# Kernel tuning notes

Measured on AMD Instinct MI355X. Metric: run time of the kernel, lower is better.

## Reference

```python
import jax
import jax.numpy as jnp
import numpy as np
from jax import lax

DIM = 512
B, T = 8, 2048
DT = 1.0
DT_REF = 1.0
MAX_GROWTH = 0.3


def _xavier(key, shape):
    fan_in, fan_out = shape[1], shape[0]
    lim = float(np.sqrt(6.0 / (fan_in + fan_out)))
    return jax.random.uniform(key, shape, jnp.float32, -lim, lim)


def setup_inputs() -> dict:
    key = jax.random.key(0)
    ks = jax.random.split(key, 10)
    D = DIM
    return {
        "x": jax.random.normal(ks[0], (B, T, D), jnp.float32),
        # ComplexSVDTransform params (U basis is unused by the transform matrix)
        "v_raw_re": jax.random.normal(ks[1], (D, D), jnp.float32) * 0.02,
        "v_raw_im": jax.random.normal(ks[2], (D, D), jnp.float32) * 0.02,
        "log_sigma": jnp.zeros((D,), jnp.float32),
        "dft_weight": jnp.zeros((), jnp.float32),
        # GlobalFluxTracker params (gate_net only used in forward_step; not here)
        "decay_re": jax.random.normal(ks[3], (D,), jnp.float32) * 0.1 - 1.0,
        "decay_im": jax.random.normal(ks[4], (D,), jnp.float32) * 0.1,
        "mix_w": _xavier(ks[5], (2 * D, 2 * D)),
        "mix_b": jnp.zeros((2 * D,), jnp.float32),
        "proj_w": _xavier(ks[6], (2 * D, 2 * D)),
        "proj_b": jnp.zeros((2 * D,), jnp.float32),
        # TemporalPropagator eigenvalue params
        "lam_re": jax.random.normal(ks[7], (D,), jnp.float32) * 0.01,
        "lam_im": jax.random.normal(ks[8], (D,), jnp.float32) * 0.1,
    }


def _cayley(raw_re, raw_im):
    # Q = (I + A_skew)^{-1} (I - A_skew), A_skew = A - A^H
    A = raw_re + 1j * raw_im
    A_skew = A - A.conj().T
    I = jnp.eye(A.shape[0], dtype=A.dtype)
    return jnp.linalg.solve(I + A_skew, I - A_skew)


def _transform_matrix(v_raw_re, v_raw_im, log_sigma, dft_weight):
    V = _cayley(v_raw_re, v_raw_im)
    S = jnp.exp(log_sigma)
    d = v_raw_re.shape[0]
    n = jnp.arange(d, dtype=jnp.float32)
    k = n[:, None]
    dft = jnp.exp(-2j * jnp.pi * (n * k) / d) / jnp.sqrt(jnp.asarray(d, jnp.float32))
    alpha = jax.nn.sigmoid(dft_weight).astype(jnp.complex64)
    V_scaled = V * S[None, :].astype(V.dtype)  # V @ diag(S)
    return V_scaled * (1.0 - alpha) + dft.astype(jnp.complex64) * alpha


def _scan_combine(c1, c2):
    # s_t = a_t * s_{t-1} + b_t  -> associative combine (later element is c2)
    a1, b1 = c1
    a2, b2 = c2
    return (a1 * a2, b1 * a2 + b2)


def reference(x, v_raw_re, v_raw_im, log_sigma, dft_weight,
              decay_re, decay_im, mix_w, mix_b, proj_w, proj_b,
              lam_re, lam_im):
    D = x.shape[-1]
    # --- encode ---
    W = _transform_matrix(v_raw_re, v_raw_im, log_sigma, dft_weight)  # [D,D] complex
    h = jnp.einsum('btd,de->bte', x.astype(jnp.complex64), W)  # [B,T,D] complex
    # --- flux tracker operators ---
    decay = jax.nn.sigmoid(decay_re) + 1j * decay_im  # [D]
    x_cat = jnp.concatenate([h.real, h.imag], axis=-1)  # [B,T,2D]
    x_in = x_cat @ mix_w.T + mix_b
    x_re, x_im = x_in[..., :D], x_in[..., D:]
    X = x_re + 1j * x_im  # forcing [B,T,D]
    A = jnp.broadcast_to(decay.astype(jnp.complex64), h.shape)  # [B,T,D]
    # --- complex diagonal SSM recurrence via parallel scan ---
    _, states = lax.associative_scan(_scan_combine, (A, X.astype(jnp.complex64)), axis=1)
    # --- project states to source ---
    s_cat = jnp.concatenate([states.real, states.imag], axis=-1)
    s_out = s_cat @ proj_w.T + proj_b
    source = s_out[..., :D] + 1j * s_out[..., D:]
    # --- closed-form transition operators ---
    lam = jnp.clip(lam_re, -MAX_GROWTH, MAX_GROWTH) + 1j * lam_im  # [D]
    exp_arg = lam * (DT / DT_REF)
    t_decay = jnp.exp(exp_arg)
    lam_safe = lam + 1e-8 * jnp.sign(lam.real + 1e-12)
    forcing = (jnp.exp(exp_arg) - 1.0) / lam_safe
    h_out = h * t_decay + source * forcing  # [B,T,D]
    # --- decode ---
    W_inv = jnp.linalg.inv(W)
    x_out = jnp.einsum('btd,de->bte', h_out, W_inv)
    return x_out.real


if __name__ == "__main__":
    out = reference(**setup_inputs())
    print(out.shape, out.dtype)
```

## Files before the change

### kernel.cpp

```cpp
#include <hip/hip_runtime.h>
#include <hip/hip_bf16.h>

typedef unsigned short u16;
typedef _Float16 f16x8 __attribute__((ext_vector_type(8)));
typedef float f32x4 __attribute__((ext_vector_type(4)));

#define DEV __device__ __forceinline__

DEV u16 f2h(float f) { _Float16 h = (_Float16)f; u16 u; __builtin_memcpy(&u, &h, 2); return u; }
DEV float h2f(u16 u) { _Float16 h; __builtin_memcpy(&h, &u, 2); return (float)h; }
DEV void splitf(float v, u16& hi, u16& lo) { hi = f2h(v); lo = f2h(v - h2f(hi)); }
DEV float sigm(float x) { return 1.f / (1.f + __expf(-x)); }
DEV void gload16(const u16* g, u16* l) {
  __builtin_amdgcn_global_load_lds((const __attribute__((address_space(1))) void*)g,
                                   (__attribute__((address_space(3))) void*)l, 16, 0, 0);
}

static const int TT = 2048;

static const size_t OFF_AUGF   = 0;
static const size_t OFF_AUG    = OFF_AUGF   + (size_t)512*512*8;
static const size_t OFF_BINV   = OFF_AUG    + (size_t)512*512*16;
static const size_t OFF_PIV    = OFF_BINV   + (size_t)64*64*16;
static const size_t OFF_MCOPY  = OFF_PIV    + (size_t)64*512*16;
static const size_t OFF_TAB    = OFF_MCOPY  + (size_t)512*64*16;
static const size_t OFF_WCATH  = OFF_TAB    + (size_t)512*32;
static const size_t OFF_WCATL  = OFF_WCATH  + (size_t)512*1024*2;
static const size_t OFF_MIXH   = OFF_WCATL  + (size_t)512*1024*2;
static const size_t OFF_MIXL   = OFF_MIXH   + (size_t)1024*1024*2;
static const size_t OFF_PROJH  = OFF_MIXL   + (size_t)1024*1024*2;
static const size_t OFF_PROJL  = OFF_PROJH  + (size_t)1024*1024*2;
static const size_t OFF_B1TH   = OFF_PROJL  + (size_t)1024*1024*2;
static const size_t OFF_B1TL   = OFF_B1TH   + (size_t)512*1024*2;
static const size_t OFF_B2TH   = OFF_B1TL   + (size_t)512*1024*2;
static const size_t OFF_B2TL   = OFF_B2TH   + (size_t)512*1024*2;
static const size_t OFF_BTMIXH = OFF_B2TL   + (size_t)512*1024*2;
static const size_t OFF_BTMIXL = OFF_BTMIXH + (size_t)1024*512*2;
static const size_t OFF_BTFH   = OFF_BTMIXL + (size_t)1024*512*2;
static const size_t OFF_BTFL   = OFF_BTFH   + (size_t)512*1536*2;
static const size_t OFF_BIAS2  = OFF_BTFL   + (size_t)512*1536*2;
static const size_t OFF_CARRY  = OFF_BIAS2  + (size_t)512*4;
static const size_t OFF_PREF   = OFF_CARRY  + (size_t)4096*16*8;
static const size_t OFF_XINF   = OFF_PREF   + (size_t)4096*16*8;
static const size_t OFF_ACATH  = OFF_XINF   + (size_t)16384*1024*4;
static const size_t OFF_ACATL  = OFF_ACATH  + (size_t)16384*1536*2;

__global__ __launch_bounds__(256) void k_split_f32(const float* __restrict__ s, u16* __restrict__ dh,
                                                   u16* __restrict__ dl, int n4) {
  int g = blockIdx.x * 256 + threadIdx.x;
  if (g >= n4) return;
  float4 v = ((const float4*)s)[g];
  ushort4 h, l;
  splitf(v.x, h.x, l.x); splitf(v.y, h.y, l.y); splitf(v.z, h.z, l.z); splitf(v.w, h.w, l.w);
  ((ushort4*)dh)[g] = h;
  ((ushort4*)dl)[g] = l;
}

__global__ __launch_bounds__(256) void k_x_to_acat(const float* __restrict__ x, u16* __restrict__ ah,
                                                   u16* __restrict__ al) {
  int g = blockIdx.x * 256 + threadIdx.x;
  if (g >= 2097152) return;
  float4 v = ((const float4*)x)[g];
  int idx = g * 4;
  int row = idx >> 9, col = idx & 511;
  ushort4 h, l;
  splitf(v.x, h.x, l.x); splitf(v.y, h.y, l.y); splitf(v.z, h.z, l.z); splitf(v.w, h.w, l.w);
  *(ushort4*)(ah + (size_t)row*1536 + col) = h;
  *(ushort4*)(al + (size_t)row*1536 + col) = l;
}

__global__ __launch_bounds__(256) void k_transpose_1024(const float* __restrict__ in, u16* __restrict__ oh,
                                                        u16* __restrict__ ol) {
  __shared__ float s[64][65];
  int lx = threadIdx.x & 63, ly = threadIdx.x >> 6;
#pragma unroll
  for (int i = 0; i < 16; ++i) {
    int c = blockIdx.y*64 + ly*16 + i;
    s[ly*16 + i][lx] = in[(size_t)c*1024 + blockIdx.x*64 + lx];
  }
  __syncthreads();
#pragma unroll
  for (int i = 0; i < 16; ++i) {
    int j = blockIdx.x*64 + ly*16 + i;
    u16 h, l; splitf(s[lx][ly*16 + i], h, l);
    oh[(size_t)j*1024 + blockIdx.y*64 + lx] = h;
    ol[(size_t)j*1024 + blockIdx.y*64 + lx] = l;
  }
}

__global__ __launch_bounds__(256) void k_build_aug_f(const float* __restrict__ vre, const float* __restrict__ vim,
                                                     float2* __restrict__ aug) {
  int g = blockIdx.x * 256 + threadIdx.x;
  if (g >= 512*512) return;
  int i = g >> 9, j = g & 511;
  float sre = vre[i*512 + j] - vre[j*512 + i];
  float sim = vim[i*512 + j] + vim[j*512 + i];
  float idd = (i == j) ? 1.f : 0.f;
  aug[g] = make_float2(idd + sre, sim);
}

template<typename T2, typename TR>
__global__ __launch_bounds__(1024) void gj_inv64_p(const T2* __restrict__ AUG, T2* __restrict__ BINV,
                                                   T2* __restrict__ MCOPY, int k0) {
  if (blockIdx.x > 0) {
    int b = blockIdx.x - 1;
    for (int l = threadIdx.x; l < 4096; l += 1024) {
      int rr = l >> 6, cc = l & 63;
      MCOPY[(size_t)(b*64 + rr)*64 + cc] = AUG[(size_t)(b*64 + rr)*512 + k0 + cc];
    }
    return;
  }
  __shared__ T2 mcol[2][64];
  __shared__ T2 praw[2][68];
  const int tid = threadIdx.x;
  const int r = tid >> 4, q = tid & 15;
  T2 a[4];
  const T2* src = AUG + (size_t)(k0 + r)*512 + k0 + q*4;
#pragma unroll
  for (int jj = 0; jj < 4; ++jj) a[jj] = src[jj];
  if (q == 0) mcol[0][r] = a[0];
  if (r == 0) {
#pragma unroll
    for (int jj = 0; jj < 4; ++jj) { int j = q*4 + jj; praw[0][j + (j >> 4)] = a[jj]; }
  }
  __syncthreads();
  for (int p = 0; p < 64; ++p) {
    const int bu = p & 1;
    T2 pd = praw[bu][p + (p >> 4)];
    TR inv = TR(1) / (pd.x*pd.x + pd.y*pd.y);
    T2 pinv; pinv.x = pd.x*inv; pinv.y = -pd.y*inv;
    T2 mraw = mcol[bu][r];
    T2 g; g.x = mraw.x*pinv.x - mraw.y*pinv.y; g.y = mraw.x*pinv.y + mraw.y*pinv.x;
    if (r == p) {
#pragma unroll
      for (int jj = 0; jj < 4; ++jj) {
        int j = q*4 + jj;
        T2 v;
        if (j == p) v = pinv;
        else { T2 pr = praw[bu][j + (j >> 4)]; v.x = pr.x*pinv.x - pr.y*pinv.y; v.y = pr.x*pinv.y + pr.y*pinv.x; }
        a[jj] = v;
      }
    } else {
#pragma unroll
      for (int jj = 0; jj < 4; ++jj) {
        int j = q*4 + jj;
        if (j == p) { a[jj].x = -g.x; a[jj].y = -g.y; }
        else {
          T2 pr = praw[bu][j + (j >> 4)];
          a[jj].x -= g.x*pr.x - g.y*pr.y;
          a[jj].y -= g.x*pr.y + g.y*pr.x;
        }
      }
    }
    if (p < 63) {
      const int nbu = bu ^ 1;
      if (q == ((p + 1) >> 2)) {
        const int loc = (p + 1) & 3;
#pragma unroll
        for (int jj = 0; jj < 4; ++jj) if (jj == loc) mcol[nbu][r] = a[jj];
      }
      if (r == p + 1) {
#pragma unroll
        for (int jj = 0; jj < 4; ++jj) { int j = q*4 + jj; praw[nbu][j + (j >> 4)] = a[jj]; }
      }
    }
    __syncthreads();
  }
  T2* dst = BINV + (size_t)r*64 + q*4;
#pragma unroll
  for (int jj = 0; jj < 4; ++jj) dst[jj] = a[jj];
}

template<typename T2>
__global__ __launch_bounds__(256) void gj_trans_t(const T2* __restrict__ AUG, const T2* __restrict__ BINV,
                                                  T2* __restrict__ PIV, int k0, int s) {
  __shared__ T2 binv[64][16];
  int tid = threadIdx.x;
  int cj = blockIdx.x + (blockIdx.x >= s ? 1 : 0);
  int col = cj*64 + (tid & 63);
  int rsub = tid >> 6;
  T2 acc[16];
#pragma unroll
  for (int i = 0; i < 16; ++i) { acc[i].x = 0; acc[i].y = 0; }
  for (int kc = 0; kc < 4; ++kc) {
    for (int l = tid; l < 1024; l += 256) {
      int rr = l >> 4, cc = l & 15;
      binv[rr][cc] = BINV[(size_t)rr*64 + kc*16 + cc];
    }
    __syncthreads();
#pragma unroll 4
    for (int kk = 0; kk < 16; ++kk) {
      T2 av = AUG[(size_t)(k0 + kc*16 + kk)*512 + col];
#pragma unroll
      for (int i = 0; i < 16; ++i) {
        T2 bv = binv[rsub*16 + i][kk];
        acc[i].x += bv.x*av.x - bv.y*av.y;
        acc[i].y += bv.x*av.y + bv.y*av.x;
      }
    }
    __syncthreads();
  }
#pragma unroll
  for (int i = 0; i < 16; ++i) PIV[(size_t)(rsub*16 + i)*512 + col] = acc[i];
}

template<typename T2>
__global__ __launch_bounds__(256) void gj_update_t(T2* __restrict__ AUG, const T2* __restrict__ PIV,
                                                   const T2* __restrict__ BINV, const T2* __restrict__ MCOPY,
                                                   int k0) {
  __shared__ T2 mult[16][64];
  __shared__ T2 pivc[16][64];
  int tid = threadIdx.x;
  int rb = blockIdx.y;
  int cj = blockIdx.x;
  const int s = k0 >> 6;
  const bool ispiv = (cj == s);
  int colBase = cj*64;
  for (int l = tid; l < 1024; l += 256) {
    int rr = l >> 6, kk = l & 63;
    mult[rr][kk] = MCOPY[(size_t)(rb*16 + rr)*64 + kk];
  }
  int ccl = tid & 63, rsub = tid >> 6;
  int col = colBase + ccl;
  T2 acc[4];
  if (ispiv) {
#pragma unroll
    for (int i = 0; i < 4; ++i) { acc[i].x = 0; acc[i].y = 0; }
  } else {
#pragma unroll
    for (int i = 0; i < 4; ++i) acc[i] = AUG[(size_t)(rb*16 + rsub*4 + i)*512 + col];
  }
  for (int kc = 0; kc < 4; ++kc) {
    for (int l = tid; l < 1024; l += 256) {
      int rr = l >> 6, cc = l & 63;
      pivc[rr][cc] = ispiv ? BINV[(size_t)(kc*16 + rr)*64 + cc]
                           : PIV[(size_t)(kc*16 + rr)*512 + colBase + cc];
    }
    __syncthreads();
#pragma unroll 4
    for (int k2 = 0; k2 < 16; ++k2) {
      T2 pv = pivc[k2][ccl];
#pragma unroll
      for (int i = 0; i < 4; ++i) {
        T2 m = mult[rsub*4 + i][kc*16 + k2];
        acc[i].x -= m.x*pv.x - m.y*pv.y;
        acc[i].y -= m.x*pv.y + m.y*pv.x;
      }
    }
    __syncthreads();
  }
#pragma unroll
  for (int i = 0; i < 4; ++i) {
    int gr = rb*16 + rsub*4 + i;
    T2 o = acc[i];
    if (gr >= k0 && gr < k0 + 64) {
      o = ispiv ? BINV[(size_t)(gr - k0)*64 + ccl] : PIV[(size_t)(gr - k0)*512 + col];
    }
    AUG[(size_t)gr*512 + col] = o;
  }
}

__global__ __launch_bounds__(256) void k_build_w(const float2* __restrict__ augf, const float* __restrict__ lsig,
                                                 const float* __restrict__ dw, double2* __restrict__ w64,
                                                 u16* __restrict__ wch, u16* __restrict__ wcl) {
  int g = blockIdx.x * 256 + threadIdx.x;
  if (g >= 512*512) return;
  int k = g >> 9, j = g & 511;
  float2 Z = augf[(size_t)k*512 + j];
  double Vre = 2.0*(double)Z.x - ((k == j) ? 1.0 : 0.0);
  double Vim = 2.0*(double)Z.y;
  double S = exp((double)lsig[j]);
  double al = 1.0 / (1.0 + exp(-(double)dw[0]));
  double sc = S * (1.0 - al);
  const float n2pi = (float)(-2.0 * 3.14159265358979323846);
  float nk = (float)(k * j);
  float ph32 = (n2pi * nk) / 512.0f;
  double sn, cs; sincos((double)ph32, &sn, &cs);
  float snf = (float)sn, csf = (float)cs;
  float rsq = sqrtf(512.0f);
  float dre = csf / rsq;
  float dimv = snf / rsq;
  double2 w = make_double2(Vre*sc + (double)dre*al, Vim*sc + (double)dimv*al);
  w64[(size_t)k*512 + j] = w;
  u16 h, l;
  splitf((float)w.x, h, l);
  wch[(size_t)k*1024 + j] = h;  wcl[(size_t)k*1024 + j] = l;
  splitf((float)w.y, h, l);
  wch[(size_t)k*1024 + 512 + j] = h;  wcl[(size_t)k*1024 + 512 + j] = l;
}

__global__ __launch_bounds__(256) void k_const512(const float* __restrict__ lamre, const float* __restrict__ lamim,
                                                  double4* __restrict__ tab) {
  int g = blockIdx.x * 256 + threadIdx.x;
  if (g >= 512) return;
  double lr = fmin(fmax((double)lamre[g], -0.3), 0.3);
  double li = (double)lamim[g];
  double e = exp(lr);
  double sn, cs; sincos(li, &sn, &cs);
  double tdre = e*cs, tdim = e*sn;
  double sgn = (lr + 1e-12) >= 0.0 ? 1.0 : -1.0;
  double lsr = lr + 1e-8*sgn, lsi = li;
  double numr = tdre - 1.0, numi = tdim;
  double idn = 1.0 / (lsr*lsr + lsi*lsi);
  double fr = (numr*lsr + numi*lsi)*idn;
  double fi = (numi*lsr - numr*lsi)*idn;
  tab[g] = make_double4(tdre, tdim, fr, fi);
}

__global__ __launch_bounds__(256) void k_build_tb(const double2* __restrict__ winv, const double4* __restrict__ tab,
                                                  u16* __restrict__ b1h, u16* __restrict__ b1l,
                                                  u16* __restrict__ b2h, u16* __restrict__ b2l) {
  int g = blockIdx.x * 256 + threadIdx.x;
  if (g >= 512*512) return;
  int e = g & 511, m = g >> 9;
  double2 wv = winv[(size_t)m*512 + e];
  double4 tb = tab[m];
  double twre = tb.x*wv.x - tb.y*wv.y, twim = tb.x*wv.y + tb.y*wv.x;
  double fwre = tb.z*wv.x - tb.w*wv.y, fwim = tb.z*wv.y + tb.w*wv.x;
  u16 h, l;
  splitf((float)twre, h, l);  b1h[(size_t)e*1024 + m] = h;        b1l[(size_t)e*1024 + m] = l;
  splitf((float)-twim, h, l); b1h[(size_t)e*1024 + 512 + m] = h;  b1l[(size_t)e*1024 + 512 + m] = l;
  splitf((float)fwre, h, l);  b2h[(size_t)e*1024 + m] = h;        b2l[(size_t)e*1024 + m] = l;
  splitf((float)-fwim, h, l); b2h[(size_t)e*1024 + 512 + m] = h;  b2l[(size_t)e*1024 + 512 + m] = l;
}

__global__ __launch_bounds__(256) void k_bias2(const double2* __restrict__ winv, const double4* __restrict__ tab,
                                               const float* __restrict__ projb, float* __restrict__ bias2) {
  int e = blockIdx.x;
  int t = threadIdx.x;
  double acc = 0.0;
  for (int d = t; d < 512; d += 256) {
    double2 wv = winv[(size_t)d*512 + e];
    double4 tb = tab[d];
    double fwre = tb.z*wv.x - tb.w*wv.y;
    double fwim = tb.z*wv.y + tb.w*wv.x;
    acc += (double)projb[d]*fwre - (double)projb[512 + d]*fwim;
  }
#pragma unroll
  for (int off = 32; off; off >>= 1) acc += __shfl_down(acc, off, 64);
  __shared__ double red[4];
  if ((t & 63) == 0) red[t >> 6] = acc;
  __syncthreads();
  if (t == 0) bias2[e] = (float)(red[0] + red[1] + red[2] + red[3]);
}

template<int K, int NOUT, int EPI, int LDA, int LDO>
__global__ __launch_bounds__(256) void gemm3(const u16* __restrict__ Ah, const u16* __restrict__ Al,
                                             const u16* __restrict__ Bh, const u16* __restrict__ Bl,
                                             u16* __restrict__ outH, u16* __restrict__ outL,
                                             float* __restrict__ outF, const float* __restrict__ bias) {
  __shared__ alignas(16) u16 Ash[128*64];
  __shared__ alignas(16) u16 Asl[128*64];
  __shared__ alignas(16) u16 Bsh[128*64];
  __shared__ alignas(16) u16 Bsl[128*64];
  const int tid = threadIdx.x;
  const int lane = tid & 63, wid = tid >> 6;
  const int wr = wid >> 1, wc = wid & 1;
  const int nwg = gridDim.x * gridDim.y;
  const int flatb = blockIdx.y * gridDim.x + blockIdx.x;
  const int chunk = nwg >> 3;
  const int swz = (flatb & 7) * chunk + (flatb >> 3);
  const int rowTile = (swz / gridDim.x) * 128;
  const int colTile = (swz % gridDim.x) * 128;
  f32x4 zz = {0.f, 0.f, 0.f, 0.f};
  f32x4 acc[4][4];
#pragma unroll
  for (int m = 0; m < 4; ++m)
#pragma unroll
    for (int n = 0; n < 4; ++n) acc[m][n] = zz;

  const int KT = K / 64;
  for (int kt = 0; kt < KT; ++kt) {
    const int k0 = kt * 64;
    __syncthreads();
#pragma unroll
    for (int i = 0; i < 4; ++i) {
      int flat = i*256 + tid;
      int ar = flat >> 3;
      int as = (flat & 7) ^ (ar & 7);
      size_t aoff = (size_t)(rowTile + ar)*LDA + (k0 + as*8);
      size_t boff = (size_t)(colTile + ar)*K   + (k0 + as*8);
      int lb = (i*256 + (tid & ~63)) * 8;
      gload16(Ah + aoff, Ash + lb);
      gload16(Al + aoff, Asl + lb);
      gload16(Bh + boff, Bsh + lb);
      gload16(Bl + boff, Bsl + lb);
    }
    __syncthreads();
#pragma unroll
    for (int ks = 0; ks < 2; ++ks) {
      f16x8 afh[4], afl[4], bfh[4], bfl[4];
#pragma unroll
      for (int m = 0; m < 4; ++m) {
        int row = wr*64 + m*16 + (lane & 15);
        int off = row*128 + (((ks*4 + (lane >> 4)) ^ (row & 7)) << 4);
        afh[m] = *(const f16x8*)((const char*)Ash + off);
        afl[m] = *(const f16x8*)((const char*)Asl + off);
      }
#pragma unroll
      for (int n = 0; n < 4; ++n) {
        int row = wc*64 + n*16 + (lane & 15);
        int off = row*128 + (((ks*4 + (lane >> 4)) ^ (row & 7)) << 4);
        bfh[n] = *(const f16x8*)((const char*)Bsh + off);
        bfl[n] = *(const f16x8*)((const char*)Bsl + off);
      }
#pragma unroll
      for (int m = 0; m < 4; ++m)
#pragma unroll
        for (int n = 0; n < 4; ++n) {
          acc[m][n] = __builtin_amdgcn_mfma_f32_16x16x32_f16(afl[m], bfh[n], acc[m][n], 0, 0, 0);
          acc[m][n] = __builtin_amdgcn_mfma_f32_16x16x32_f16(afh[m], bfl[n], acc[m][n], 0, 0, 0);
          acc[m][n] = __builtin_amdgcn_mfma_f32_16x16x32_f16(afh[m], bfh[n], acc[m][n], 0, 0, 0);
        }
    }
  }
  const int colBase = colTile + wc*64;
  const int rowBase = rowTile + wr*64 + (lane >> 4)*4;
#pragma unroll
  for (int n = 0; n < 4; ++n) {
    int col = colBase + n*16 + (lane & 15);
    float bv = (EPI >= 2) ? bias[col] : 0.f;
#pragma unroll
    for (int m = 0; m < 4; ++m) {
#pragma unroll
      for (int j = 0; j < 4; ++j) {
        int row = rowBase + m*16 + j;
        float v = acc[m][n][j] + bv;
        if (EPI >= 2) {
          outF[(size_t)row*LDO + col] = v;
        } else {
          u16 h, l; splitf(v, h, l);
          outH[(size_t)row*LDO + col] = h;
          outL[(size_t)row*LDO + col] = l;
        }
      }
    }
  }
}

__global__ __launch_bounds__(256) void k_scan1(const float* __restrict__ xin, const float* __restrict__ dre_,
                                               const float* __restrict__ dim_, float2* __restrict__ carry) {
  int g = blockIdx.x * 256 + threadIdx.x;
  int d = g & 511; int rr = g >> 9; int b = rr & 7; int c = rr >> 3;
  float dre = sigm(dre_[d]);
  float dim = dim_[d];
  size_t base = ((size_t)(b*TT + c*128))*1024 + d;
  float sre = 0.f, sim = 0.f;
  for (int t = 0; t < 128; ++t) {
    float xre = xin[base];
    float xim = xin[base + 512];
    float nre = dre*sre - dim*sim + xre;
    float nim = dre*sim + dim*sre + xim;
    sre = nre; sim = nim;
    base += 1024;
  }
  carry[((size_t)(b*512 + d))*16 + c] = make_float2(sre, sim);
}

__global__ __launch_bounds__(256) void k_scan2(const float* __restrict__ dre_, const float* __restrict__ dim_,
                                               const float2* __restrict__ carry, float2* __restrict__ pref) {
  int g = blockIdx.x * 256 + threadIdx.x;
  int d = g & 511; int b = g >> 9;
  float dre = sigm(dre_[d]);
  float dim = dim_[d];
  float are = dre, aim = dim;
#pragma unroll
  for (int i = 0; i < 7; ++i) { float nr = are*are - aim*aim; float ni = 2.f*are*aim; are = nr; aim = ni; }
  float sre = 0.f, sim = 0.f;
  size_t base = ((size_t)(b*512 + d))*16;
  for (int c = 0; c < 16; ++c) {
    pref[base + c] = make_float2(sre, sim);
    float2 cr = carry[base + c];
    float nr = are*sre - aim*sim + cr.x;
    float ni = are*sim + aim*sre + cr.y;
    sre = nr; sim = ni;
  }
}

__global__ __launch_bounds__(256) void k_scan3(const float* __restrict__ xin, const float* __restrict__ dre_,
                                               const float* __restrict__ dim_, const float2* __restrict__ pref,
                                               u16* __restrict__ ah, u16* __restrict__ al) {
  int g = blockIdx.x * 256 + threadIdx.x;
  int d = g & 511; int rr = g >> 9; int b = rr & 7; int c = rr >> 3;
  float dre = sigm(dre_[d]);
  float dim = dim_[d];
  float2 p0 = pref[((size_t)(b*512 + d))*16 + c];
  float sre = p0.x, sim = p0.y;
  size_t base  = ((size_t)(b*TT + c*128))*1024 + d;
  size_t base2 = ((size_t)(b*TT + c*128))*1536 + d;
  for (int t = 0; t < 128; ++t) {
    float xre = xin[base];
    float xim = xin[base + 512];
    float nre = dre*sre - dim*sim + xre;
    float nim = dre*sim + dim*sre + xim;
    sre = nre; sim = nim;
    u16 h, l;
    splitf(sre, h, l); ah[base2 + 512]  = h; al[base2 + 512]  = l;
    splitf(sim, h, l); ah[base2 + 1024] = h; al[base2 + 1024] = l;
    base += 1024; base2 += 1536;
  }
}

extern "C" void kernel_launch(void* const* d_in, const int* in_sizes, int n_in,
                              void* d_out, int out_size, void* d_ws, size_t ws_size,
                              hipStream_t stream) {
  (void)in_sizes; (void)n_in; (void)out_size; (void)ws_size;
  const float* x     = (const float*)d_in[0];
  const float* vre   = (const float*)d_in[1];
  const float* vim   = (const float*)d_in[2];
  const float* lsig  = (const float*)d_in[3];
  const float* dw    = (const float*)d_in[4];
  const float* decre = (const float*)d_in[5];
  const float* decim = (const float*)d_in[6];
  const float* mixw  = (const float*)d_in[7];
  const float* mixb  = (const float*)d_in[8];
  const float* projw = (const float*)d_in[9];
  const float* projb = (const float*)d_in[10];
  const float* lamre = (const float*)d_in[11];
  const float* lamim = (const float*)d_in[12];
  float* out = (float*)d_out;
  char* ws = (char*)d_ws;

  float2*  AUGF   = (float2*)(ws + OFF_AUGF);
  double2* AUG    = (double2*)(ws + OFF_AUG);
  double2* BINV   = (double2*)(ws + OFF_BINV);
  float2*  BINVF  = (float2*)(ws + OFF_BINV);
  double2* PIV    = (double2*)(ws + OFF_PIV);
  float2*  PIVF   = (float2*)(ws + OFF_PIV);
  double2* MCOPY  = (double2*)(ws + OFF_MCOPY);
  float2*  MCOPYF = (float2*)(ws + OFF_MCOPY);
  double4* TAB    = (double4*)(ws + OFF_TAB);
  u16*    WCATH  = (u16*)(ws + OFF_WCATH);
  u16*    WCATL  = (u16*)(ws + OFF_WCATL);
  u16*    MIXH   = (u16*)(ws + OFF_MIXH);
  u16*    MIXL   = (u16*)(ws + OFF_MIXL);
  u16*    PROJH  = (u16*)(ws + OFF_PROJH);
  u16*    PROJL  = (u16*)(ws + OFF_PROJL);
  u16*    B1TH   = (u16*)(ws + OFF_B1TH);
  u16*    B1TL   = (u16*)(ws + OFF_B1TL);
  u16*    B2TH   = (u16*)(ws + OFF_B2TH);
  u16*    B2TL   = (u16*)(ws + OFF_B2TL);
  u16*    BTMIXH = (u16*)(ws + OFF_BTMIXH);
  u16*    BTMIXL = (u16*)(ws + OFF_BTMIXL);
  u16*    BTFH   = (u16*)(ws + OFF_BTFH);
  u16*    BTFL   = (u16*)(ws + OFF_BTFL);
  float*  BIAS2  = (float*)(ws + OFF_BIAS2);
  float2* CARRY  = (float2*)(ws + OFF_CARRY);
  float2* PREF   = (float2*)(ws + OFF_PREF);
  float*  XINF   = (float*)(ws + OFF_XINF);
  u16*    ACATH  = (u16*)(ws + OFF_ACATH);
  u16*    ACATL  = (u16*)(ws + OFF_ACATL);

  k_const512<<<2, 256, 0, stream>>>(lamre, lamim, TAB);
  k_x_to_acat<<<8192, 256, 0, stream>>>(x, ACATH, ACATL);
  k_split_f32<<<1024, 256, 0, stream>>>(mixw, MIXH, MIXL, 262144);
  k_transpose_1024<<<dim3(16, 16), 256, 0, stream>>>(projw, PROJH, PROJL);

  k_build_aug_f<<<1024, 256, 0, stream>>>(vre, vim, AUGF);
  for (int s = 0; s < 8; ++s) {
    int k0 = s * 64;
    gj_inv64_p<float2, float><<<9, 1024, 0, stream>>>(AUGF, BINVF, MCOPYF, k0);
    gj_trans_t<float2><<<7, 256, 0, stream>>>(AUGF, BINVF, PIVF, k0, s);
    gj_update_t<float2><<<dim3(8, 32), 256, 0, stream>>>(AUGF, PIVF, BINVF, MCOPYF, k0);
  }
  k_build_w<<<1024, 256, 0, stream>>>(AUGF, lsig, dw, AUG, WCATH, WCATL);

  for (int s = 0; s < 8; ++s) {
    int k0 = s * 64;
    gj_inv64_p<double2, double><<<9, 1024, 0, stream>>>(AUG, BINV, MCOPY, k0);
    gj_trans_t<double2><<<7, 256, 0, stream>>>(AUG, BINV, PIV, k0, s);
    gj_update_t<double2><<<dim3(8, 32), 256, 0, stream>>>(AUG, PIV, BINV, MCOPY, k0);
  }

  k_build_tb<<<1024, 256, 0, stream>>>(AUG, TAB, B1TH, B1TL, B2TH, B2TL);
  k_bias2<<<512, 256, 0, stream>>>(AUG, TAB, projb, BIAS2);
  gemm3<1024, 512, 0, 1024, 1536><<<dim3(4, 4), 256, 0, stream>>>(B1TH, B1TL, WCATH, WCATL, BTFH, BTFL, nullptr, nullptr);
  gemm3<1024, 1024, 0, 1024, 1536><<<dim3(8, 4), 256, 0, stream>>>(B2TH, B2TL, PROJH, PROJL, BTFH + 512, BTFL + 512, nullptr, nullptr);
  gemm3<1024, 512, 0, 1024, 512><<<dim3(4, 8), 256, 0, stream>>>(MIXH, MIXL, WCATH, WCATL, BTMIXH, BTMIXL, nullptr, nullptr);

  gemm3<512, 1024, 3, 1536, 1024><<<dim3(8, 128), 256, 0, stream>>>(ACATH, ACATL, BTMIXH, BTMIXL, nullptr, nullptr, XINF, mixb);

  k_scan1<<<256, 256, 0, stream>>>(XINF, decre, decim, CARRY);
  k_scan2<<<16, 256, 0, stream>>>(decre, decim, CARRY, PREF);
  k_scan3<<<256, 256, 0, stream>>>(XINF, decre, decim, PREF, ACATH, ACATL);

  gemm3<1536, 512, 2, 1536, 512><<<dim3(4, 128), 256, 0, stream>>>(ACATH, ACATL, BTFH, BTFL, nullptr, nullptr, out, BIAS2);
}
```

Measured before the change: 2.341 ms.

## Fuse blocked Gauss-Jordan steps into one kernel per step with lookahead inversion

Replaces the three kernels per Gauss-Jordan block step (pivot-block inversion, pivot-row transform, trailing update) with a single fused step kernel. Each step computes the transformed pivot row in shared memory and applies the update. The block holding the next pivot tile inverts it in place, and next-step copies are written to double-buffered scratch. This cuts kernel launches from 24 to about 9 per inversion and removes serialized tiny kernels, but one block now does a serial 64-step inversion at the tail of each step.

```diff
diff --git a/kernel.cpp b/kernel.cpp
--- a/kernel.cpp
+++ b/kernel.cpp
@@ -20,10 +20,10 @@
 
 static const size_t OFF_AUGF   = 0;
 static const size_t OFF_AUG    = OFF_AUGF   + (size_t)512*512*8;
-static const size_t OFF_BINV   = OFF_AUG    + (size_t)512*512*16;
-static const size_t OFF_PIV    = OFF_BINV   + (size_t)64*64*16;
-static const size_t OFF_MCOPY  = OFF_PIV    + (size_t)64*512*16;
-static const size_t OFF_TAB    = OFF_MCOPY  + (size_t)512*64*16;
+static const size_t OFF_BINV2  = OFF_AUG    + (size_t)512*512*16;
+static const size_t OFF_MCOPY2 = OFF_BINV2  + (size_t)2*64*64*16;
+static const size_t OFF_RCOPY2 = OFF_MCOPY2 + (size_t)2*512*64*16;
+static const size_t OFF_TAB    = OFF_RCOPY2 + (size_t)2*64*512*16;
 static const size_t OFF_WCATH  = OFF_TAB    + (size_t)512*32;
 static const size_t OFF_WCATL  = OFF_WCATH  + (size_t)512*1024*2;
 static const size_t OFF_MIXH   = OFF_WCATL  + (size_t)512*1024*2;
@@ -100,36 +100,21 @@
 }
 
 template<typename T2, typename TR>
-__global__ __launch_bounds__(1024) void gj_inv64_p(const T2* __restrict__ AUG, T2* __restrict__ BINV,
-                                                   T2* __restrict__ MCOPY, int k0) {
-  if (blockIdx.x > 0) {
-    int b = blockIdx.x - 1;
-    for (int l = threadIdx.x; l < 4096; l += 1024) {
-      int rr = l >> 6, cc = l & 63;
-      MCOPY[(size_t)(b*64 + rr)*64 + cc] = AUG[(size_t)(b*64 + rr)*512 + k0 + cc];
-    }
-    return;
-  }
-  __shared__ T2 mcol[2][64];
-  __shared__ T2 praw[2][68];
+DEV void inv64_reg(T2* a, T2* mcol , T2* praw , T2* __restrict__ BINVout) {
   const int tid = threadIdx.x;
   const int r = tid >> 4, q = tid & 15;
-  T2 a[4];
-  const T2* src = AUG + (size_t)(k0 + r)*512 + k0 + q*4;
-#pragma unroll
-  for (int jj = 0; jj < 4; ++jj) a[jj] = src[jj];
-  if (q == 0) mcol[0][r] = a[0];
+  if (q == 0) mcol[0*64 + r] = a[0];
   if (r == 0) {
 #pragma unroll
-    for (int jj = 0; jj < 4; ++jj) { int j = q*4 + jj; praw[0][j + (j >> 4)] = a[jj]; }
+    for (int jj = 0; jj < 4; ++jj) { int j = q*4 + jj; praw[0*68 + j + (j >> 4)] = a[jj]; }
   }
   __syncthreads();
   for (int p = 0; p < 64; ++p) {
     const int bu = p & 1;
-    T2 pd = praw[bu][p + (p >> 4)];
+    T2 pd = praw[bu*68 + p + (p >> 4)];
     TR inv = TR(1) / (pd.x*pd.x + pd.y*pd.y);
     T2 pinv; pinv.x = pd.x*inv; pinv.y = -pd.y*inv;
-    T2 mraw = mcol[bu][r];
+    T2 mraw = mcol[bu*64 + r];
     T2 g; g.x = mraw.x*pinv.x - mraw.y*pinv.y; g.y = mraw.x*pinv.y + mraw.y*pinv.x;
     if (r == p) {
 #pragma unroll
@@ -137,7 +122,7 @@
         int j = q*4 + jj;
         T2 v;
         if (j == p) v = pinv;
-        else { T2 pr = praw[bu][j + (j >> 4)]; v.x = pr.x*pinv.x - pr.y*pinv.y; v.y = pr.x*pinv.y + pr.y*pinv.x; }
+        else { T2 pr = praw[bu*68 + j + (j >> 4)]; v.x = pr.x*pinv.x - pr.y*pinv.y; v.y = pr.x*pinv.y + pr.y*pinv.x; }
         a[jj] = v;
       }
     } else {
@@ -146,7 +131,7 @@
         int j = q*4 + jj;
         if (j == p) { a[jj].x = -g.x; a[jj].y = -g.y; }
         else {
-          T2 pr = praw[bu][j + (j >> 4)];
+          T2 pr = praw[bu*68 + j + (j >> 4)];
           a[jj].x -= g.x*pr.x - g.y*pr.y;
           a[jj].y -= g.x*pr.y + g.y*pr.x;
         }
@@ -157,106 +142,121 @@
       if (q == ((p + 1) >> 2)) {
         const int loc = (p + 1) & 3;
 #pragma unroll
-        for (int jj = 0; jj < 4; ++jj) if (jj == loc) mcol[nbu][r] = a[jj];
+        for (int jj = 0; jj < 4; ++jj) if (jj == loc) mcol[nbu*64 + r] = a[jj];
       }
       if (r == p + 1) {
 #pragma unroll
-        for (int jj = 0; jj < 4; ++jj) { int j = q*4 + jj; praw[nbu][j + (j >> 4)] = a[jj]; }
+        for (int jj = 0; jj < 4; ++jj) { int j = q*4 + jj; praw[nbu*68 + j + (j >> 4)] = a[jj]; }
       }
     }
     __syncthreads();
   }
-  T2* dst = BINV + (size_t)r*64 + q*4;
-#pragma unroll
-  for (int jj = 0; jj < 4; ++jj) dst[jj] = a[jj];
-}
-
-template<typename T2>
-__global__ __launch_bounds__(256) void gj_trans_t(const T2* __restrict__ AUG, const T2* __restrict__ BINV,
-                                                  T2* __restrict__ PIV, int k0, int s) {
-  __shared__ T2 binv[64][16];
+#pragma unroll
+  for (int jj = 0; jj < 4; ++jj) BINVout[(size_t)r*64 + q*4 + jj] = a[jj];
+}
+
+template<typename T2, typename TR>
+__global__ __launch_bounds__(1024) void gj_prep(const T2* __restrict__ AUG, T2* __restrict__ BINV2,
+                                                T2* __restrict__ MCOPY2, T2* __restrict__ RCOPY2) {
+  __shared__ T2 mcol[2*64];
+  __shared__ T2 praw[2*68];
   int tid = threadIdx.x;
-  int cj = blockIdx.x + (blockIdx.x >= s ? 1 : 0);
-  int col = cj*64 + (tid & 63);
-  int rsub = tid >> 6;
-  T2 acc[16];
-#pragma unroll
-  for (int i = 0; i < 16; ++i) { acc[i].x = 0; acc[i].y = 0; }
-  for (int kc = 0; kc < 4; ++kc) {
-    for (int l = tid; l < 1024; l += 256) {
-      int rr = l >> 4, cc = l & 15;
-      binv[rr][cc] = BINV[(size_t)rr*64 + kc*16 + cc];
-    }
-    __syncthreads();
-#pragma unroll 4
-    for (int kk = 0; kk < 16; ++kk) {
-      T2 av = AUG[(size_t)(k0 + kc*16 + kk)*512 + col];
-#pragma unroll
-      for (int i = 0; i < 16; ++i) {
-        T2 bv = binv[rsub*16 + i][kk];
-        acc[i].x += bv.x*av.x - bv.y*av.y;
-        acc[i].y += bv.x*av.y + bv.y*av.x;
-      }
-    }
-    __syncthreads();
-  }
-#pragma unroll
-  for (int i = 0; i < 16; ++i) PIV[(size_t)(rsub*16 + i)*512 + col] = acc[i];
-}
-
-template<typename T2>
-__global__ __launch_bounds__(256) void gj_update_t(T2* __restrict__ AUG, const T2* __restrict__ PIV,
-                                                   const T2* __restrict__ BINV, const T2* __restrict__ MCOPY,
-                                                   int k0) {
-  __shared__ T2 mult[16][64];
-  __shared__ T2 pivc[16][64];
-  int tid = threadIdx.x;
-  int rb = blockIdx.y;
-  int cj = blockIdx.x;
-  const int s = k0 >> 6;
-  const bool ispiv = (cj == s);
-  int colBase = cj*64;
-  for (int l = tid; l < 1024; l += 256) {
-    int rr = l >> 6, kk = l & 63;
-    mult[rr][kk] = MCOPY[(size_t)(rb*16 + rr)*64 + kk];
-  }
-  int ccl = tid & 63, rsub = tid >> 6;
-  int col = colBase + ccl;
-  T2 acc[4];
-  if (ispiv) {
-#pragma unroll
-    for (int i = 0; i < 4; ++i) { acc[i].x = 0; acc[i].y = 0; }
+  int b = blockIdx.x;
+  if (b == 0) {
+    const int r = tid >> 4, q = tid & 15;
+    T2 a[4];
+#pragma unroll
+    for (int jj = 0; jj < 4; ++jj) a[jj] = AUG[(size_t)r*512 + q*4 + jj];
+    inv64_reg<T2, TR>(a, mcol, praw, BINV2);
+  } else if (b <= 8) {
+    int boff = (b - 1) * 64;
+    for (int l = tid; l < 4096; l += 1024) {
+      int rr = l >> 6, cc = l & 63;
+      MCOPY2[(size_t)(boff + rr)*64 + cc] = AUG[(size_t)(boff + rr)*512 + cc];
+    }
   } else {
-#pragma unroll
-    for (int i = 0; i < 4; ++i) acc[i] = AUG[(size_t)(rb*16 + rsub*4 + i)*512 + col];
-  }
-  for (int kc = 0; kc < 4; ++kc) {
-    for (int l = tid; l < 1024; l += 256) {
+    int coff = (b - 9) * 64;
+    for (int l = tid; l < 4096; l += 1024) {
       int rr = l >> 6, cc = l & 63;
-      pivc[rr][cc] = ispiv ? BINV[(size_t)(kc*16 + rr)*64 + cc]
-                           : PIV[(size_t)(kc*16 + rr)*512 + colBase + cc];
-    }
-    __syncthreads();
-#pragma unroll 4
-    for (int k2 = 0; k2 < 16; ++k2) {
-      T2 pv = pivc[k2][ccl];
-#pragma unroll
-      for (int i = 0; i < 4; ++i) {
-        T2 m = mult[rsub*4 + i][kc*16 + k2];
-        acc[i].x -= m.x*pv.x - m.y*pv.y;
-        acc[i].y -= m.x*pv.y + m.y*pv.x;
-      }
-    }
-    __syncthreads();
-  }
-#pragma unroll
-  for (int i = 0; i < 4; ++i) {
-    int gr = rb*16 + rsub*4 + i;
-    T2 o = acc[i];
-    if (gr >= k0 && gr < k0 + 64) {
-      o = ispiv ? BINV[(size_t)(gr - k0)*64 + ccl] : PIV[(size_t)(gr - k0)*512 + col];
-    }
-    AUG[(size_t)gr*512 + col] = o;
+      RCOPY2[(size_t)rr*512 + coff + cc] = AUG[(size_t)rr*512 + coff + cc];
+    }
+  }
+}
+
+template<typename T2, typename TR>
+__global__ __launch_bounds__(1024) void gj_step(T2* __restrict__ AUG, T2* __restrict__ BINV2,
+                                                T2* __restrict__ MCOPY2, T2* __restrict__ RCOPY2, int s) {
+  __shared__ T2 Psh[64*64];
+  __shared__ T2 mcol[2*64];
+  __shared__ T2 praw[2*68];
+  const int cj = blockIdx.x, rg = blockIdx.y;
+  const int par = s & 1;
+  const T2* __restrict__ BINV = BINV2 + (size_t)par*4096;
+  const T2* __restrict__ MC   = MCOPY2 + (size_t)par*512*64;
+  const T2* __restrict__ RC   = RCOPY2 + (size_t)par*64*512;
+  T2* __restrict__ BINVn = BINV2 + (size_t)(par ^ 1)*4096;
+  T2* __restrict__ MCn   = MCOPY2 + (size_t)(par ^ 1)*512*64;
+  T2* __restrict__ RCn   = RCOPY2 + (size_t)(par ^ 1)*64*512;
+  const int tid = threadIdx.x;
+  if (cj == s) {
+    for (int l = tid; l < 4096; l += 1024) Psh[l] = BINV[l];
+  } else {
+    const int k = tid >> 4, q4 = (tid & 15) * 4;
+    T2 p[4];
+#pragma unroll
+    for (int jj = 0; jj < 4; ++jj) { p[jj].x = 0; p[jj].y = 0; }
+    for (int t = 0; t < 64; ++t) {
+      T2 b = BINV[k*64 + t];
+#pragma unroll
+      for (int jj = 0; jj < 4; ++jj) {
+        T2 rv = RC[(size_t)t*512 + cj*64 + q4 + jj];
+        p[jj].x += b.x*rv.x - b.y*rv.y;
+        p[jj].y += b.x*rv.y + b.y*rv.x;
+      }
+    }
+#pragma unroll
+    for (int jj = 0; jj < 4; ++jj) Psh[k*64 + q4 + jj] = p[jj];
+  }
+  __syncthreads();
+  const int r = tid >> 4, q4 = (tid & 15) * 4;
+  const int grow = rg*64 + r;
+  T2 a[4];
+  if (rg == s) {
+#pragma unroll
+    for (int jj = 0; jj < 4; ++jj) a[jj] = Psh[r*64 + q4 + jj];
+  } else {
+    if (cj == s) {
+#pragma unroll
+      for (int jj = 0; jj < 4; ++jj) { a[jj].x = 0; a[jj].y = 0; }
+    } else {
+#pragma unroll
+      for (int jj = 0; jj < 4; ++jj) a[jj] = AUG[(size_t)grow*512 + cj*64 + q4 + jj];
+    }
+    for (int k = 0; k < 64; ++k) {
+      T2 m = MC[(size_t)grow*64 + k];
+#pragma unroll
+      for (int jj = 0; jj < 4; ++jj) {
+        T2 pv = Psh[k*64 + q4 + jj];
+        a[jj].x -= m.x*pv.x - m.y*pv.y;
+        a[jj].y -= m.x*pv.y + m.y*pv.x;
+      }
+    }
+  }
+#pragma unroll
+  for (int jj = 0; jj < 4; ++jj) AUG[(size_t)grow*512 + cj*64 + q4 + jj] = a[jj];
+  if (s < 7) {
+    if (cj == s + 1) {
+#pragma unroll
+      for (int jj = 0; jj < 4; ++jj) MCn[(size_t)grow*64 + q4 + jj] = a[jj];
+    }
+    if (rg == s + 1) {
+#pragma unroll
+      for (int jj = 0; jj < 4; ++jj) RCn[(size_t)r*512 + cj*64 + q4 + jj] = a[jj];
+    }
+    if (cj == s + 1 && rg == s + 1) {
+      __syncthreads();
+      inv64_reg<T2, TR>(a, mcol, praw, BINVn);
+    }
   }
 }
 
@@ -521,15 +521,15 @@
   float* out = (float*)d_out;
   char* ws = (char*)d_ws;
 
-  float2*  AUGF   = (float2*)(ws + OFF_AUGF);
-  double2* AUG    = (double2*)(ws + OFF_AUG);
-  double2* BINV   = (double2*)(ws + OFF_BINV);
-  float2*  BINVF  = (float2*)(ws + OFF_BINV);
-  double2* PIV    = (double2*)(ws + OFF_PIV);
-  float2*  PIVF   = (float2*)(ws + OFF_PIV);
-  double2* MCOPY  = (double2*)(ws + OFF_MCOPY);
-  float2*  MCOPYF = (float2*)(ws + OFF_MCOPY);
-  double4* TAB    = (double4*)(ws + OFF_TAB);
+  float2*  AUGF    = (float2*)(ws + OFF_AUGF);
+  double2* AUG     = (double2*)(ws + OFF_AUG);
+  double2* BINV2   = (double2*)(ws + OFF_BINV2);
+  float2*  BINV2F  = (float2*)(ws + OFF_BINV2);
+  double2* MCOPY2  = (double2*)(ws + OFF_MCOPY2);
+  float2*  MCOPY2F = (float2*)(ws + OFF_MCOPY2);
+  double2* RCOPY2  = (double2*)(ws + OFF_RCOPY2);
+  float2*  RCOPY2F = (float2*)(ws + OFF_RCOPY2);
+  double4* TAB     = (double4*)(ws + OFF_TAB);
   u16*    WCATH  = (u16*)(ws + OFF_WCATH);
   u16*    WCATL  = (u16*)(ws + OFF_WCATL);
   u16*    MIXH   = (u16*)(ws + OFF_MIXH);
@@ -557,20 +557,14 @@
   k_transpose_1024<<<dim3(16, 16), 256, 0, stream>>>(projw, PROJH, PROJL);
 
   k_build_aug_f<<<1024, 256, 0, stream>>>(vre, vim, AUGF);
-  for (int s = 0; s < 8; ++s) {
-    int k0 = s * 64;
-    gj_inv64_p<float2, float><<<9, 1024, 0, stream>>>(AUGF, BINVF, MCOPYF, k0);
-    gj_trans_t<float2><<<7, 256, 0, stream>>>(AUGF, BINVF, PIVF, k0, s);
-    gj_update_t<float2><<<dim3(8, 32), 256, 0, stream>>>(AUGF, PIVF, BINVF, MCOPYF, k0);
-  }
+  gj_prep<float2, float><<<17, 1024, 0, stream>>>(AUGF, BINV2F, MCOPY2F, RCOPY2F);
+  for (int s = 0; s < 8; ++s)
+    gj_step<float2, float><<<dim3(8, 8), 1024, 0, stream>>>(AUGF, BINV2F, MCOPY2F, RCOPY2F, s);
   k_build_w<<<1024, 256, 0, stream>>>(AUGF, lsig, dw, AUG, WCATH, WCATL);
 
-  for (int s = 0; s < 8; ++s) {
-    int k0 = s * 64;
-    gj_inv64_p<double2, double><<<9, 1024, 0, stream>>>(AUG, BINV, MCOPY, k0);
-    gj_trans_t<double2><<<7, 256, 0, stream>>>(AUG, BINV, PIV, k0, s);
-    gj_update_t<double2><<<dim3(8, 32), 256, 0, stream>>>(AUG, PIV, BINV, MCOPY, k0);
-  }
+  gj_prep<double2, double><<<17, 1024, 0, stream>>>(AUG, BINV2, MCOPY2, RCOPY2);
+  for (int s = 0; s < 8; ++s)
+    gj_step<double2, double><<<dim3(8, 8), 1024, 0, stream>>>(AUG, BINV2, MCOPY2, RCOPY2, s);
 
   k_build_tb<<<1024, 256, 0, stream>>>(AUG, TAB, B1TH, B1TL, B2TH, B2TL);
   k_bias2<<<512, 256, 0, stream>>>(AUG, TAB, projb, BIAS2);
```

Result: slower. 3.984 ms (+70.2%).
